# Kernel tuning notes

Hardware: AMD Instinct MI355X
Metric: run time of the kernel (lower is better)

Reference implementation:

```python
import jax, jax.numpy as jnp
import numpy as np

N = 262144
FC = 256
XYZ_FREQ, DIR_FREQ = 10, 4
IN_XYZ = 3 + 3 * 2 * XYZ_FREQ  # 63
IN_DIR = 3 + 3 * 2 * DIR_FREQ  # 27
SKIP = 4


def posenc(p, n_freqs):
    bands = 2.0 ** jnp.arange(n_freqs, dtype=p.dtype)          # [F]
    xb = p[..., None, :] * bands[:, None]                       # [N, F, 3]
    sc = jnp.stack([jnp.sin(xb), jnp.cos(xb)], axis=-2)         # [N, F, 2, 3]
    return jnp.concatenate([p, sc.reshape(p.shape[0], n_freqs * 6)], axis=-1)


def setup_inputs() -> dict:
    key = jax.random.key(0)
    ks = jax.random.split(key, 32)
    s = 0.05
    inp = {"x": jax.random.normal(ks[0], (N, 6), jnp.float32)}
    dims_in = [IN_XYZ] + [FC + IN_XYZ if i == SKIP else FC for i in range(1, 8)]
    for i in range(8):
        inp[f"w{i}"] = jax.random.normal(ks[1 + i], (dims_in[i], FC), jnp.float32) * s
        inp[f"b{i}"] = jnp.zeros((FC,), jnp.float32)
    inp["w_final"] = jax.random.normal(ks[10], (FC, FC), jnp.float32) * s
    inp["b_final"] = jnp.zeros((FC,), jnp.float32)
    inp["w_sigma"] = jax.random.normal(ks[11], (FC, 1), jnp.float32) * s
    inp["b_sigma"] = jnp.zeros((1,), jnp.float32)
    inp["w_rgb1"] = jax.random.normal(ks[12], (FC + IN_DIR, FC // 2), jnp.float32) * s
    inp["b_rgb1"] = jnp.zeros((FC // 2,), jnp.float32)
    inp["w_rgb2"] = jax.random.normal(ks[13], (FC // 2, 3), jnp.float32) * s
    inp["b_rgb2"] = jnp.zeros((3,), jnp.float32)
    return inp


def reference(x, w0, b0, w1, b1, w2, b2, w3, b3, w4, b4, w5, b5, w6, b6, w7, b7,
              w_final, b_final, w_sigma, b_sigma, w_rgb1, b_rgb1, w_rgb2, b_rgb2):
    input_xyz = posenc(x[:, :3], XYZ_FREQ)   # [N, 63]
    input_dir = posenc(x[:, 3:], DIR_FREQ)   # [N, 27]
    ws = [w0, w1, w2, w3, w4, w5, w6, w7]
    bs = [b0, b1, b2, b3, b4, b5, b6, b7]
    h = input_xyz
    for i in range(8):
        if i == SKIP:
            h = jnp.concatenate([input_xyz, h], axis=-1)
        h = jax.nn.relu(h @ ws[i] + bs[i])
    sigma = h @ w_sigma + b_sigma                               # [N, 1]
    final = h @ w_final + b_final                               # [N, 256]
    dir_enc = jnp.concatenate([final, input_dir], axis=-1)      # [N, 283]
    hidden = jax.nn.relu(dir_enc @ w_rgb1 + b_rgb1)
    rgb = jax.nn.sigmoid(hidden @ w_rgb2 + b_rgb2)              # [N, 3]
    return jnp.concatenate([rgb, sigma], axis=-1)               # [N, 4]
```

## Files before the change

kernel.cpp:

```cpp
#include <hip/hip_runtime.h>
#include <hip/hip_fp16.h>
#include <stdint.h>

typedef unsigned int   uint32;
typedef unsigned short ushort_t;
typedef _Float16 half8   __attribute__((ext_vector_type(8)));
typedef float    floatx4 __attribute__((ext_vector_type(4)));

#define DEVINL __device__ __forceinline__

#define N_FRAGS 1172

DEVINL int fragoff(int row, int f) {
    return (f >> 5)*2048 + (row >> 4)*512 + ((f >> 3) & 3)*128 + (row & 15)*8 + (f & 7);
}

__device__ __align__(16) ushort_t g_ws[(size_t)N_FRAGS * 512];

DEVINL ushort_t f2h_u(float v) { return __half_as_ushort(__float2half(v)); }

DEVINL uint4 make_frag_qword(const float* __restrict__ W, int Kr, int Nr,
                             int skip63, int kt, int nt, int q, int cc)
{
    const int n = nt*16 + cc;
    uint32 pk[4];
    #pragma unroll
    for (int jj = 0; jj < 4; ++jj) {
        ushort_t h2[2];
        #pragma unroll
        for (int e = 0; e < 2; ++e) {
            const int k = kt*32 + q*8 + jj*2 + e;
            float v = 0.f;
            if (n < Nr) {
                if (skip63) {
                    if (k != 63) { const int rr = (k < 63) ? k : (k - 1); v = W[(size_t)rr*Nr + n]; }
                } else if (k < Kr) {
                    v = W[(size_t)k*Nr + n];
                }
            }
            h2[e] = f2h_u(v);
        }
        pk[jj] = (uint32)h2[0] | ((uint32)h2[1] << 16);
    }
    return make_uint4(pk[0], pk[1], pk[2], pk[3]);
}

__global__ __launch_bounds__(256) void prep_weights(
    const float* __restrict__ w0, const float* __restrict__ w1,
    const float* __restrict__ w2, const float* __restrict__ w3,
    const float* __restrict__ w4, const float* __restrict__ w5,
    const float* __restrict__ w6, const float* __restrict__ w7,
    const float* __restrict__ wf, const float* __restrict__ wsig,
    const float* __restrict__ wr1, const float* __restrict__ wr2)
{
    int gid  = blockIdx.x * 256 + threadIdx.x;
    int frag = gid >> 6;
    if (frag >= N_FRAGS) return;
    int lane = gid & 63;

    constexpr int foff[13] = {0,32,160,288,416,576,704,832,960,1088,1096,1168,1172};
    int t = 0;
    #pragma unroll
    for (int i = 1; i <= 11; ++i) if (frag >= foff[i]) t = i;

    const float* W; int fo, ntc, Kr, Nr;
    switch (t) {
        case 0:  W = w0;   fo = 0;    ntc = 16; Kr = 63;  Nr = 256; break;
        case 1:  W = w1;   fo = 32;   ntc = 16; Kr = 256; Nr = 256; break;
        case 2:  W = w2;   fo = 160;  ntc = 16; Kr = 256; Nr = 256; break;
        case 3:  W = w3;   fo = 288;  ntc = 16; Kr = 256; Nr = 256; break;
        case 4:  W = w4;   fo = 416;  ntc = 16; Kr = 319; Nr = 256; break;
        case 5:  W = w5;   fo = 576;  ntc = 16; Kr = 256; Nr = 256; break;
        case 6:  W = w6;   fo = 704;  ntc = 16; Kr = 256; Nr = 256; break;
        case 7:  W = w7;   fo = 832;  ntc = 16; Kr = 256; Nr = 256; break;
        case 8:  W = wf;   fo = 960;  ntc = 16; Kr = 256; Nr = 256; break;
        case 9:  W = wsig; fo = 1088; ntc = 1;  Kr = 256; Nr = 1;   break;
        case 10: W = wr1;  fo = 1096; ntc = 8;  Kr = 283; Nr = 128; break;
        default: W = wr2;  fo = 1168; ntc = 1;  Kr = 128; Nr = 3;   break;
    }
    int fl = frag - fo;
    int nt = fl % ntc;
    int kt = fl / ntc;
    uint4 pk = make_frag_qword(W, Kr, Nr, (t == 4) ? 1 : 0, kt, nt,
                               lane >> 4, lane & 15);
    *(uint4*)(g_ws + (size_t)frag*512 + lane*8) = pk;
}

template <int NT_W, int KT, int KT_SPLIT, int NTT>
DEVINL void run_layer(const ushort_t* __restrict__ wsrc,
                      const ushort_t* __restrict__ in0,
                      const ushort_t* __restrict__ in1,
                      int lane, int nt_lo,
                      const floatx4 (&binit)[NT_W], floatx4 (&acc)[4][NT_W])
{
    half8 bfr[2][4];
    half8 afr[2][NT_W];

    auto loadk = [&](int kt, int buf) {
        const ushort_t* bb = ((kt < KT_SPLIT) ? in0 + kt*2048
                                              : in1 + (kt - KT_SPLIT)*2048) + lane*8;
        #pragma unroll
        for (int rt = 0; rt < 4; ++rt)
            bfr[buf][rt] = *(const half8*)(bb + rt*512);
        const ushort_t* wb = wsrc + (size_t)(kt*NTT + nt_lo)*512 + lane*8;
        #pragma unroll
        for (int nt = 0; nt < NT_W; ++nt)
            afr[buf][nt] = *(const half8*)(wb + nt*512);
    };

    loadk(0, 0);
    #pragma unroll
    for (int kt = 0; kt < KT; ++kt) {
        const int cur = kt & 1;
        if (kt + 1 < KT) loadk(kt + 1, cur ^ 1);
        #pragma unroll
        for (int nt = 0; nt < NT_W; ++nt)
            #pragma unroll
            for (int rt = 0; rt < 4; ++rt)
                acc[rt][nt] = __builtin_amdgcn_mfma_f32_16x16x32_f16(
                    afr[cur][nt], bfr[cur][rt],
                    (kt == 0) ? binit[nt] : acc[rt][nt], 0, 0, 0);
    }
}

template <int NT_W, bool RELU>
DEVINL void epilogue_h(floatx4 (&acc)[4][NT_W], int nt_lo,
                       ushort_t* __restrict__ dsth, int q, int cc)
{
    #pragma unroll
    for (int rt = 0; rt < 4; ++rt) {
        #pragma unroll
        for (int nt = 0; nt < NT_W; ++nt) {
            const int ng = nt_lo + nt;
            floatx4 v = acc[rt][nt];
            if (RELU) {
                v.x = fmaxf(v.x, 0.f); v.y = fmaxf(v.y, 0.f);
                v.z = fmaxf(v.z, 0.f); v.w = fmaxf(v.w, 0.f);
            }
            uint2 u;
            u.x = __builtin_bit_cast(uint32, __builtin_amdgcn_cvt_pkrtz(v.x, v.y));
            u.y = __builtin_bit_cast(uint32, __builtin_amdgcn_cvt_pkrtz(v.z, v.w));
            const int dst = (ng >> 1)*2048 + rt*512
                          + (((2*ng + (q >> 1)) & 3)*16 + cc)*8 + (q & 1)*4;
            *(uint2*)(dsth + dst) = u;
        }
    }
}

__global__ __launch_bounds__(256, 3) void nerf_fused(
    const float* __restrict__ x,
    const float* __restrict__ b0, const float* __restrict__ b1,
    const float* __restrict__ b2, const float* __restrict__ b3,
    const float* __restrict__ b4, const float* __restrict__ b5,
    const float* __restrict__ b6, const float* __restrict__ b7,
    const float* __restrict__ bf, const float* __restrict__ bsig,
    const float* __restrict__ br1, const float* __restrict__ br2,
    float* __restrict__ out)
{
    __shared__ __align__(16) ushort_t shh[8*2048];
    __shared__ __align__(16) ushort_t shx[2*2048];
    __shared__ __align__(16) ushort_t shd[2048];

    const int tid  = threadIdx.x;
    const int wave = tid >> 6, lane = tid & 63;
    const int q = lane >> 4, cc = lane & 15;
    const int r0 = blockIdx.x * 64;
    const ushort_t* ws = g_ws;

    {
        const int r = lane;
        const float* xr = x + (size_t)(r0 + r)*6;
        for (int j = wave; j < 42; j += 4) {
            if (j < 30) {
                int f = j/3, a = j%3;
                float v = xr[a] * (float)(1 << f);
                shx[fragoff(r, 3 + f*6 + a)]     = f2h_u(sinf(v));
                shx[fragoff(r, 3 + f*6 + 3 + a)] = f2h_u(cosf(v));
            } else {
                int jj = j - 30, f = jj/3, a = jj%3;
                float v = xr[3+a] * (float)(1 << f);
                shd[fragoff(r, 3 + f*6 + a)]     = f2h_u(sinf(v));
                shd[fragoff(r, 3 + f*6 + 3 + a)] = f2h_u(cosf(v));
            }
        }
        if (wave == 0) {
            #pragma unroll
            for (int a = 0; a < 3; ++a) {
                shx[fragoff(r, a)] = f2h_u(xr[a]);
                shd[fragoff(r, a)] = f2h_u(xr[3+a]);
            }
            shx[fragoff(r, 63)] = 0;
            #pragma unroll
            for (int kq = 27; kq < 32; ++kq) shd[fragoff(r, kq)] = 0;
        }
    }
    __syncthreads();

    const float* BS[8] = {b0,b1,b2,b3,b4,b5,b6,b7};
    const int WO[8] = {0,16384,81920,147456,212992,294912,360448,425984};
    const int nt_lo4 = wave * 4;
    const floatx4 vz = {0.f, 0.f, 0.f, 0.f};

    floatx4 acc[4][4];
    floatx4 bl[4];

    #pragma unroll
    for (int nt = 0; nt < 4; ++nt)
        bl[nt] = *(const floatx4*)(b0 + (nt_lo4 + nt)*16 + q*4);
    run_layer<4,2,2,16>(ws + WO[0], shx, shx, lane, nt_lo4, bl, acc);
    epilogue_h<4,true>(acc, nt_lo4, shh, q, cc);
    __syncthreads();

    #pragma unroll
    for (int l = 1; l < 8; ++l) {
        #pragma unroll
        for (int nt = 0; nt < 4; ++nt)
            bl[nt] = *(const floatx4*)(BS[l] + (nt_lo4 + nt)*16 + q*4);
        if (l == 4)
            run_layer<4,10,2,16>(ws + WO[4], shx, shh, lane, nt_lo4, bl, acc);
        else
            run_layer<4,8,8,16>(ws + WO[l], shh, shh, lane, nt_lo4, bl, acc);
        __syncthreads();
        epilogue_h<4,true>(acc, nt_lo4, shh, q, cc);
        __syncthreads();
    }

    if (wave == 0) {
        floatx4 sacc[4][1];
        const floatx4 bz[1] = {vz};
        run_layer<1,8,8,1>(ws + 557056, shh, shh, lane, 0, bz, sacc);
        if (q == 0) {
            const float bs_ = bsig[0];
            #pragma unroll
            for (int rt = 0; rt < 4; ++rt)
                out[(size_t)(r0 + rt*16 + cc)*4 + 3] = sacc[rt][0].x + bs_;
        }
    }

    #pragma unroll
    for (int nt = 0; nt < 4; ++nt)
        bl[nt] = *(const floatx4*)(bf + (nt_lo4 + nt)*16 + q*4);
    run_layer<4,8,8,16>(ws + 491520, shh, shh, lane, nt_lo4, bl, acc);
    __syncthreads();
    epilogue_h<4,false>(acc, nt_lo4, shh, q, cc);
    __syncthreads();

    {
        floatx4 racc[4][2];
        floatx4 bl2[2];
        #pragma unroll
        for (int nt = 0; nt < 2; ++nt)
            bl2[nt] = *(const floatx4*)(br1 + (wave*2 + nt)*16 + q*4);
        run_layer<2,9,8,8>(ws + 561152, shh, shd, lane, wave*2, bl2, racc);
        __syncthreads();
        epilogue_h<2,true>(racc, wave*2, shh, q, cc);
        __syncthreads();
    }

    if (wave == 0) {
        floatx4 cacc[4][1];
        const floatx4 bz[1] = {vz};
        run_layer<1,4,4,1>(ws + 598016, shh, shh, lane, 0, bz, cacc);
        if (q == 0) {
            const float c0 = br2[0], c1 = br2[1], c2 = br2[2];
            #pragma unroll
            for (int rt = 0; rt < 4; ++rt) {
                const size_t o = (size_t)(r0 + rt*16 + cc)*4;
                out[o+0] = 1.f/(1.f + expf(-(cacc[rt][0].x + c0)));
                out[o+1] = 1.f/(1.f + expf(-(cacc[rt][0].y + c1)));
                out[o+2] = 1.f/(1.f + expf(-(cacc[rt][0].z + c2)));
            }
        }
    }
}

extern "C" void kernel_launch(void* const* d_in, const int* in_sizes, int n_in,
                              void* d_out, int out_size, void* d_ws, size_t ws_size,
                              hipStream_t stream)
{
    const float* x  = (const float*)d_in[0];
    const float* w0 = (const float*)d_in[1];  const float* b0 = (const float*)d_in[2];
    const float* w1 = (const float*)d_in[3];  const float* b1 = (const float*)d_in[4];
    const float* w2 = (const float*)d_in[5];  const float* b2 = (const float*)d_in[6];
    const float* w3 = (const float*)d_in[7];  const float* b3 = (const float*)d_in[8];
    const float* w4 = (const float*)d_in[9];  const float* b4 = (const float*)d_in[10];
    const float* w5 = (const float*)d_in[11]; const float* b5 = (const float*)d_in[12];
    const float* w6 = (const float*)d_in[13]; const float* b6 = (const float*)d_in[14];
    const float* w7 = (const float*)d_in[15]; const float* b7 = (const float*)d_in[16];
    const float* wf = (const float*)d_in[17]; const float* bf = (const float*)d_in[18];
    const float* wsg= (const float*)d_in[19]; const float* bsg= (const float*)d_in[20];
    const float* wr1= (const float*)d_in[21]; const float* br1= (const float*)d_in[22];
    const float* wr2= (const float*)d_in[23]; const float* br2= (const float*)d_in[24];
    float* out = (float*)d_out;
    const int N = in_sizes[0] / 6;

    prep_weights<<<(N_FRAGS*64 + 255)/256, 256, 0, stream>>>(
        w0,w1,w2,w3,w4,w5,w6,w7,wf,wsg,wr1,wr2);
    nerf_fused<<<N/64, 256, 0, stream>>>(
        x, b0,b1,b2,b3,b4,b5,b6,b7, bf,bsg, br1,br2, out);
}
```

Measured before the change: 384.0 us.

## Switch MLP layers to 32x32x16 MFMA with new fragment layout

Moves every layer from 16x16x32 to 32x32x16 MFMA instructions. This changes the weight fragment packing, the shared-memory activation layout and the epilogue, which now adds the bias instead of seeding the accumulator. The direction encoding now reuses the xyz shared buffer, computed after layer 4 consumes it, which cuts LDS use and lets the launch bounds rise to 4 blocks per CU. It aims for fewer MFMA issues and fewer LDS fragment loads per FLOP, at the cost of more accumulator registers and a riskier, more intricate layout.

```diff
diff --git a/kernel.cpp b/kernel.cpp
--- a/kernel.cpp
+++ b/kernel.cpp
@@ -4,15 +4,17 @@
 
 typedef unsigned int   uint32;
 typedef unsigned short ushort_t;
-typedef _Float16 half8   __attribute__((ext_vector_type(8)));
-typedef float    floatx4 __attribute__((ext_vector_type(4)));
+typedef _Float16 half8    __attribute__((ext_vector_type(8)));
+typedef float    floatx4  __attribute__((ext_vector_type(4)));
+typedef float    floatx16 __attribute__((ext_vector_type(16)));
 
 #define DEVINL __device__ __forceinline__
 
-#define N_FRAGS 1172
+#define N_FRAGS 1184
 
 DEVINL int fragoff(int row, int f) {
-    return (f >> 5)*2048 + (row >> 4)*512 + ((f >> 3) & 3)*128 + (row & 15)*8 + (f & 7);
+    return (f >> 4)*1024 + (row >> 5)*512
+         + ((((f >> 3) & 1) << 5) + (row & 31))*8 + (f & 7);
 }
 
 __device__ __align__(16) ushort_t g_ws[(size_t)N_FRAGS * 512];
@@ -20,16 +22,16 @@
 DEVINL ushort_t f2h_u(float v) { return __half_as_ushort(__float2half(v)); }
 
 DEVINL uint4 make_frag_qword(const float* __restrict__ W, int Kr, int Nr,
-                             int skip63, int kt, int nt, int q, int cc)
-{
-    const int n = nt*16 + cc;
+                             int skip63, int kt, int nt, int s, int c)
+{
+    const int n = nt*32 + c;
     uint32 pk[4];
     #pragma unroll
     for (int jj = 0; jj < 4; ++jj) {
         ushort_t h2[2];
         #pragma unroll
         for (int e = 0; e < 2; ++e) {
-            const int k = kt*32 + q*8 + jj*2 + e;
+            const int k = kt*16 + s*8 + jj*2 + e;
             float v = 0.f;
             if (n < Nr) {
                 if (skip63) {
@@ -58,31 +60,31 @@
     if (frag >= N_FRAGS) return;
     int lane = gid & 63;
 
-    constexpr int foff[13] = {0,32,160,288,416,576,704,832,960,1088,1096,1168,1172};
+    constexpr int foff[13] = {0,32,160,288,416,576,704,832,960,1088,1104,1176,1184};
     int t = 0;
     #pragma unroll
     for (int i = 1; i <= 11; ++i) if (frag >= foff[i]) t = i;
 
     const float* W; int fo, ntc, Kr, Nr;
     switch (t) {
-        case 0:  W = w0;   fo = 0;    ntc = 16; Kr = 63;  Nr = 256; break;
-        case 1:  W = w1;   fo = 32;   ntc = 16; Kr = 256; Nr = 256; break;
-        case 2:  W = w2;   fo = 160;  ntc = 16; Kr = 256; Nr = 256; break;
-        case 3:  W = w3;   fo = 288;  ntc = 16; Kr = 256; Nr = 256; break;
-        case 4:  W = w4;   fo = 416;  ntc = 16; Kr = 319; Nr = 256; break;
-        case 5:  W = w5;   fo = 576;  ntc = 16; Kr = 256; Nr = 256; break;
-        case 6:  W = w6;   fo = 704;  ntc = 16; Kr = 256; Nr = 256; break;
-        case 7:  W = w7;   fo = 832;  ntc = 16; Kr = 256; Nr = 256; break;
-        case 8:  W = wf;   fo = 960;  ntc = 16; Kr = 256; Nr = 256; break;
-        case 9:  W = wsig; fo = 1088; ntc = 1;  Kr = 256; Nr = 1;   break;
-        case 10: W = wr1;  fo = 1096; ntc = 8;  Kr = 283; Nr = 128; break;
-        default: W = wr2;  fo = 1168; ntc = 1;  Kr = 128; Nr = 3;   break;
+        case 0:  W = w0;   fo = 0;    ntc = 8; Kr = 63;  Nr = 256; break;
+        case 1:  W = w1;   fo = 32;   ntc = 8; Kr = 256; Nr = 256; break;
+        case 2:  W = w2;   fo = 160;  ntc = 8; Kr = 256; Nr = 256; break;
+        case 3:  W = w3;   fo = 288;  ntc = 8; Kr = 256; Nr = 256; break;
+        case 4:  W = w4;   fo = 416;  ntc = 8; Kr = 319; Nr = 256; break;
+        case 5:  W = w5;   fo = 576;  ntc = 8; Kr = 256; Nr = 256; break;
+        case 6:  W = w6;   fo = 704;  ntc = 8; Kr = 256; Nr = 256; break;
+        case 7:  W = w7;   fo = 832;  ntc = 8; Kr = 256; Nr = 256; break;
+        case 8:  W = wf;   fo = 960;  ntc = 8; Kr = 256; Nr = 256; break;
+        case 9:  W = wsig; fo = 1088; ntc = 1; Kr = 256; Nr = 1;   break;
+        case 10: W = wr1;  fo = 1104; ntc = 4; Kr = 283; Nr = 128; break;
+        default: W = wr2;  fo = 1176; ntc = 1; Kr = 128; Nr = 3;   break;
     }
     int fl = frag - fo;
     int nt = fl % ntc;
     int kt = fl / ntc;
     uint4 pk = make_frag_qword(W, Kr, Nr, (t == 4) ? 1 : 0, kt, nt,
-                               lane >> 4, lane & 15);
+                               lane >> 5, lane & 31);
     *(uint4*)(g_ws + (size_t)frag*512 + lane*8) = pk;
 }
 
@@ -90,17 +92,18 @@
 DEVINL void run_layer(const ushort_t* __restrict__ wsrc,
                       const ushort_t* __restrict__ in0,
                       const ushort_t* __restrict__ in1,
-                      int lane, int nt_lo,
-                      const floatx4 (&binit)[NT_W], floatx4 (&acc)[4][NT_W])
-{
-    half8 bfr[2][4];
+                      int lane, int nt_lo, floatx16 (&acc)[2][NT_W])
+{
+    half8 bfr[2][2];
     half8 afr[2][NT_W];
+    const floatx16 vz = {0.f,0.f,0.f,0.f, 0.f,0.f,0.f,0.f,
+                         0.f,0.f,0.f,0.f, 0.f,0.f,0.f,0.f};
 
     auto loadk = [&](int kt, int buf) {
-        const ushort_t* bb = ((kt < KT_SPLIT) ? in0 + kt*2048
-                                              : in1 + (kt - KT_SPLIT)*2048) + lane*8;
-        #pragma unroll
-        for (int rt = 0; rt < 4; ++rt)
+        const ushort_t* bb = ((kt < KT_SPLIT) ? in0 + kt*1024
+                                              : in1 + (kt - KT_SPLIT)*1024) + lane*8;
+        #pragma unroll
+        for (int rt = 0; rt < 2; ++rt)
             bfr[buf][rt] = *(const half8*)(bb + rt*512);
         const ushort_t* wb = wsrc + (size_t)(kt*NTT + nt_lo)*512 + lane*8;
         #pragma unroll
@@ -116,38 +119,50 @@
         #pragma unroll
         for (int nt = 0; nt < NT_W; ++nt)
             #pragma unroll
-            for (int rt = 0; rt < 4; ++rt)
-                acc[rt][nt] = __builtin_amdgcn_mfma_f32_16x16x32_f16(
+            for (int rt = 0; rt < 2; ++rt)
+                acc[rt][nt] = __builtin_amdgcn_mfma_f32_32x32x16_f16(
                     afr[cur][nt], bfr[cur][rt],
-                    (kt == 0) ? binit[nt] : acc[rt][nt], 0, 0, 0);
+                    (kt == 0) ? vz : acc[rt][nt], 0, 0, 0);
     }
 }
 
 template <int NT_W, bool RELU>
-DEVINL void epilogue_h(floatx4 (&acc)[4][NT_W], int nt_lo,
-                       ushort_t* __restrict__ dsth, int q, int cc)
-{
-    #pragma unroll
-    for (int rt = 0; rt < 4; ++rt) {
-        #pragma unroll
-        for (int nt = 0; nt < NT_W; ++nt) {
-            const int ng = nt_lo + nt;
-            floatx4 v = acc[rt][nt];
-            if (RELU) {
-                v.x = fmaxf(v.x, 0.f); v.y = fmaxf(v.y, 0.f);
-                v.z = fmaxf(v.z, 0.f); v.w = fmaxf(v.w, 0.f);
-            }
-            uint2 u;
-            u.x = __builtin_bit_cast(uint32, __builtin_amdgcn_cvt_pkrtz(v.x, v.y));
-            u.y = __builtin_bit_cast(uint32, __builtin_amdgcn_cvt_pkrtz(v.z, v.w));
-            const int dst = (ng >> 1)*2048 + rt*512
-                          + (((2*ng + (q >> 1)) & 3)*16 + cc)*8 + (q & 1)*4;
-            *(uint2*)(dsth + dst) = u;
-        }
-    }
-}
-
-__global__ __launch_bounds__(256, 3) void nerf_fused(
+DEVINL void epilogue32(floatx16 (&acc)[2][NT_W], int nt_lo,
+                       ushort_t* __restrict__ dsth, const float* __restrict__ bias,
+                       int lane)
+{
+    const int s = lane >> 5, c = lane & 31;
+    #pragma unroll
+    for (int nt = 0; nt < NT_W; ++nt) {
+        const int n0 = (nt_lo + nt)*32;
+        floatx4 q[4];
+        #pragma unroll
+        for (int p = 0; p < 4; ++p)
+            q[p] = *(const floatx4*)(bias + n0 + 8*p + 4*s);
+        #pragma unroll
+        for (int rt = 0; rt < 2; ++rt) {
+            #pragma unroll
+            for (int r4 = 0; r4 < 16; r4 += 4) {
+                float v0 = acc[rt][nt][r4+0] + q[r4>>2][0];
+                float v1 = acc[rt][nt][r4+1] + q[r4>>2][1];
+                float v2 = acc[rt][nt][r4+2] + q[r4>>2][2];
+                float v3 = acc[rt][nt][r4+3] + q[r4>>2][3];
+                if (RELU) {
+                    v0 = fmaxf(v0, 0.f); v1 = fmaxf(v1, 0.f);
+                    v2 = fmaxf(v2, 0.f); v3 = fmaxf(v3, 0.f);
+                }
+                uint2 u;
+                u.x = __builtin_bit_cast(uint32, __builtin_amdgcn_cvt_pkrtz(v0, v1));
+                u.y = __builtin_bit_cast(uint32, __builtin_amdgcn_cvt_pkrtz(v2, v3));
+                const int dst = ((nt_lo + nt)*2 + (r4 >> 3))*1024 + rt*512
+                              + ((((r4 >> 2) & 1) << 5) + c)*8 + 4*s;
+                *(uint2*)(dsth + dst) = u;
+            }
+        }
+    }
+}
+
+__global__ __launch_bounds__(256, 4) void nerf_fused(
     const float* __restrict__ x,
     const float* __restrict__ b0, const float* __restrict__ b1,
     const float* __restrict__ b2, const float* __restrict__ b3,
@@ -157,118 +172,105 @@
     const float* __restrict__ br1, const float* __restrict__ br2,
     float* __restrict__ out)
 {
-    __shared__ __align__(16) ushort_t shh[8*2048];
-    __shared__ __align__(16) ushort_t shx[2*2048];
-    __shared__ __align__(16) ushort_t shd[2048];
+    __shared__ __align__(16) ushort_t shh[16*1024];
+    __shared__ __align__(16) ushort_t shx[4*1024];
+    ushort_t* shd = shx;
 
     const int tid  = threadIdx.x;
     const int wave = tid >> 6, lane = tid & 63;
-    const int q = lane >> 4, cc = lane & 15;
     const int r0 = blockIdx.x * 64;
     const ushort_t* ws = g_ws;
+    const int nt_lo2 = wave * 2;
 
     {
         const int r = lane;
         const float* xr = x + (size_t)(r0 + r)*6;
-        for (int j = wave; j < 42; j += 4) {
-            if (j < 30) {
+        for (int j = wave; j < 30; j += 4) {
+            int f = j/3, a = j%3;
+            float v = xr[a] * (float)(1 << f);
+            shx[fragoff(r, 3 + f*6 + a)]     = f2h_u(sinf(v));
+            shx[fragoff(r, 3 + f*6 + 3 + a)] = f2h_u(cosf(v));
+        }
+        if (wave == 0) {
+            #pragma unroll
+            for (int a = 0; a < 3; ++a) shx[fragoff(r, a)] = f2h_u(xr[a]);
+            shx[fragoff(r, 63)] = 0;
+        }
+    }
+    __syncthreads();
+
+    const float* BS[8] = {b0,b1,b2,b3,b4,b5,b6,b7};
+    const int WO[8] = {0,16384,81920,147456,212992,294912,360448,425984};
+
+    floatx16 acc[2][2];
+
+    run_layer<2,4,4,8>(ws + WO[0], shx, shx, lane, nt_lo2, acc);
+    __syncthreads();
+    epilogue32<2,true>(acc, nt_lo2, shh, b0, lane);
+    __syncthreads();
+
+    #pragma unroll
+    for (int l = 1; l < 8; ++l) {
+        if (l == 4)
+            run_layer<2,20,4,8>(ws + WO[4], shx, shh, lane, nt_lo2, acc);
+        else
+            run_layer<2,16,16,8>(ws + WO[l], shh, shh, lane, nt_lo2, acc);
+        __syncthreads();
+        if (l == 4) {
+            const int r = lane;
+            const float* xr = x + (size_t)(r0 + r)*6;
+            for (int j = wave; j < 12; j += 4) {
                 int f = j/3, a = j%3;
-                float v = xr[a] * (float)(1 << f);
-                shx[fragoff(r, 3 + f*6 + a)]     = f2h_u(sinf(v));
-                shx[fragoff(r, 3 + f*6 + 3 + a)] = f2h_u(cosf(v));
-            } else {
-                int jj = j - 30, f = jj/3, a = jj%3;
                 float v = xr[3+a] * (float)(1 << f);
                 shd[fragoff(r, 3 + f*6 + a)]     = f2h_u(sinf(v));
                 shd[fragoff(r, 3 + f*6 + 3 + a)] = f2h_u(cosf(v));
             }
-        }
-        if (wave == 0) {
-            #pragma unroll
-            for (int a = 0; a < 3; ++a) {
-                shx[fragoff(r, a)] = f2h_u(xr[a]);
-                shd[fragoff(r, a)] = f2h_u(xr[3+a]);
-            }
-            shx[fragoff(r, 63)] = 0;
-            #pragma unroll
-            for (int kq = 27; kq < 32; ++kq) shd[fragoff(r, kq)] = 0;
-        }
-    }
-    __syncthreads();
-
-    const float* BS[8] = {b0,b1,b2,b3,b4,b5,b6,b7};
-    const int WO[8] = {0,16384,81920,147456,212992,294912,360448,425984};
-    const int nt_lo4 = wave * 4;
-    const floatx4 vz = {0.f, 0.f, 0.f, 0.f};
-
-    floatx4 acc[4][4];
-    floatx4 bl[4];
-
-    #pragma unroll
-    for (int nt = 0; nt < 4; ++nt)
-        bl[nt] = *(const floatx4*)(b0 + (nt_lo4 + nt)*16 + q*4);
-    run_layer<4,2,2,16>(ws + WO[0], shx, shx, lane, nt_lo4, bl, acc);
-    epilogue_h<4,true>(acc, nt_lo4, shh, q, cc);
-    __syncthreads();
-
-    #pragma unroll
-    for (int l = 1; l < 8; ++l) {
-        #pragma unroll
-        for (int nt = 0; nt < 4; ++nt)
-            bl[nt] = *(const floatx4*)(BS[l] + (nt_lo4 + nt)*16 + q*4);
-        if (l == 4)
-            run_layer<4,10,2,16>(ws + WO[4], shx, shh, lane, nt_lo4, bl, acc);
-        else
-            run_layer<4,8,8,16>(ws + WO[l], shh, shh, lane, nt_lo4, bl, acc);
+            if (wave == 0) {
+                #pragma unroll
+                for (int a = 0; a < 3; ++a) shd[fragoff(r, a)] = f2h_u(xr[3+a]);
+                #pragma unroll
+                for (int kq = 27; kq < 32; ++kq) shd[fragoff(r, kq)] = 0;
+            }
+        }
+        epilogue32<2,true>(acc, nt_lo2, shh, BS[l], lane);
         __syncthreads();
-        epilogue_h<4,true>(acc, nt_lo4, shh, q, cc);
+    }
+
+    if (wave == 0) {
+        floatx16 sacc[2][1];
+        run_layer<1,16,16,1>(ws + 557056, shh, shh, lane, 0, sacc);
+        if (lane < 32) {
+            const float bs_ = bsig[0];
+            #pragma unroll
+            for (int rt = 0; rt < 2; ++rt)
+                out[(size_t)(r0 + rt*32 + lane)*4 + 3] = sacc[rt][0][0] + bs_;
+        }
+    }
+
+    run_layer<2,16,16,8>(ws + 491520, shh, shh, lane, nt_lo2, acc);
+    __syncthreads();
+    epilogue32<2,false>(acc, nt_lo2, shh, bf, lane);
+    __syncthreads();
+
+    {
+        floatx16 racc[2][1];
+        run_layer<1,18,16,4>(ws + 565248, shh, shd, lane, wave, racc);
         __syncthreads();
+        epilogue32<1,true>(racc, wave, shh, br1, lane);
+        __syncthreads();
     }
 
     if (wave == 0) {
-        floatx4 sacc[4][1];
-        const floatx4 bz[1] = {vz};
-        run_layer<1,8,8,1>(ws + 557056, shh, shh, lane, 0, bz, sacc);
-        if (q == 0) {
-            const float bs_ = bsig[0];
-            #pragma unroll
-            for (int rt = 0; rt < 4; ++rt)
-                out[(size_t)(r0 + rt*16 + cc)*4 + 3] = sacc[rt][0].x + bs_;
-        }
-    }
-
-    #pragma unroll
-    for (int nt = 0; nt < 4; ++nt)
-        bl[nt] = *(const floatx4*)(bf + (nt_lo4 + nt)*16 + q*4);
-    run_layer<4,8,8,16>(ws + 491520, shh, shh, lane, nt_lo4, bl, acc);
-    __syncthreads();
-    epilogue_h<4,false>(acc, nt_lo4, shh, q, cc);
-    __syncthreads();
-
-    {
-        floatx4 racc[4][2];
-        floatx4 bl2[2];
-        #pragma unroll
-        for (int nt = 0; nt < 2; ++nt)
-            bl2[nt] = *(const floatx4*)(br1 + (wave*2 + nt)*16 + q*4);
-        run_layer<2,9,8,8>(ws + 561152, shh, shd, lane, wave*2, bl2, racc);
-        __syncthreads();
-        epilogue_h<2,true>(racc, wave*2, shh, q, cc);
-        __syncthreads();
-    }
-
-    if (wave == 0) {
-        floatx4 cacc[4][1];
-        const floatx4 bz[1] = {vz};
-        run_layer<1,4,4,1>(ws + 598016, shh, shh, lane, 0, bz, cacc);
-        if (q == 0) {
+        floatx16 cacc[2][1];
+        run_layer<1,8,8,1>(ws + 602112, shh, shh, lane, 0, cacc);
+        if (lane < 32) {
             const float c0 = br2[0], c1 = br2[1], c2 = br2[2];
             #pragma unroll
-            for (int rt = 0; rt < 4; ++rt) {
-                const size_t o = (size_t)(r0 + rt*16 + cc)*4;
-                out[o+0] = 1.f/(1.f + expf(-(cacc[rt][0].x + c0)));
-                out[o+1] = 1.f/(1.f + expf(-(cacc[rt][0].y + c1)));
-                out[o+2] = 1.f/(1.f + expf(-(cacc[rt][0].z + c2)));
+            for (int rt = 0; rt < 2; ++rt) {
+                const size_t o = (size_t)(r0 + rt*32 + lane)*4;
+                out[o+0] = 1.f/(1.f + expf(-(cacc[rt][0][0] + c0)));
+                out[o+1] = 1.f/(1.f + expf(-(cacc[rt][0][1] + c1)));
+                out[o+2] = 1.f/(1.f + expf(-(cacc[rt][0][2] + c2)));
             }
         }
     }
```

Result: slower. 465.9 us (+21.3%).
